# Kernel tuning notes

Measured on AMD Instinct MI355X. Metric: run time of the kernel, lower is better.

Reference implementation:

```python
import jax, jax.numpy as jnp
import numpy as np

N_GO, N_KE, D = 8000, 2000, 16
N_LAYERS, N_TISSUE, DRUG = 3, 512, 2048
B = 256


def _scatter_add(msgs, dst, n):
    # msgs: [B, E, D] -> [B, n, D], summing messages into destination nodes
    Bm, _, d = msgs.shape
    return jnp.zeros((Bm, n, d), msgs.dtype).at[:, dst, :].add(msgs)


def setup_inputs() -> dict:
    key = jax.random.key(0)
    ks = jax.random.split(key, 20)
    inp = {
        "x": jax.random.normal(ks[0], (B, N_GO + DRUG), jnp.float32),
        "go_ke_src": jax.random.randint(ks[1], (50000,), 0, N_GO),
        "go_ke_dst": jax.random.randint(ks[2], (50000,), 0, N_KE),
        "ke_ke_src": jax.random.randint(ks[3], (20000,), 0, N_KE),
        "ke_ke_dst": jax.random.randint(ks[4], (20000,), 0, N_KE),
        "tissue": jax.random.randint(ks[5], (N_TISSUE,), 0, N_KE),
    }
    def w(k, shape, fan_in):
        return jax.random.normal(k, shape, jnp.float32) / np.sqrt(fan_in)
    inp["W_dec"] = w(ks[6], (N_GO, D), 1.0)          # per-GO scalar->vector layer
    inp["b_dec"] = jnp.zeros((N_GO, D), jnp.float32)
    inp["W_g2k"] = w(ks[7], (D, D), D)
    inp["b_g2k"] = jnp.zeros((D,), jnp.float32)
    inp["W_kk"] = w(ks[8], (N_LAYERS, D, D), D)
    inp["b_kk"] = jnp.zeros((N_LAYERS, D), jnp.float32)
    inp["w_ke"] = w(ks[9], (D,), D)                   # node readout D->1
    inp["b_ke"] = jnp.zeros((), jnp.float32)
    inp["W_bio1"] = w(ks[10], (N_TISSUE, 256), N_TISSUE)
    inp["b_bio1"] = jnp.zeros((256,), jnp.float32)
    inp["W_bio2"] = w(ks[11], (256, 128), 256)
    inp["b_bio2"] = jnp.zeros((128,), jnp.float32)
    inp["W_drug1"] = w(ks[12], (DRUG, 512), DRUG)
    inp["b_drug1"] = jnp.zeros((512,), jnp.float32)
    inp["W_drug2"] = w(ks[13], (512, 128), 512)
    inp["b_drug2"] = jnp.zeros((128,), jnp.float32)
    inp["W_pred"] = w(ks[14], (256, 1), 256)
    inp["b_pred"] = jnp.zeros((1,), jnp.float32)
    return inp


def reference(x, go_ke_src, go_ke_dst, ke_ke_src, ke_ke_dst, tissue,
              W_dec, b_dec, W_g2k, b_g2k, W_kk, b_kk, w_ke, b_ke,
              W_bio1, b_bio1, W_bio2, b_bio2,
              W_drug1, b_drug1, W_drug2, b_drug2, W_pred, b_pred):
    # go_decode_layer: per-GO scalar -> D-dim node feature
    go = jnp.tanh(x[:, :-DRUG, None] * W_dec + b_dec)          # [B, N_GO, D]
    # go2ke: gather source GO features, scatter-add into KE nodes, transform
    ke = _scatter_add(go[:, go_ke_src, :], go_ke_dst, N_KE)    # [B, N_KE, D]
    ke = jnp.tanh(ke @ W_g2k + b_g2k)
    # ke2ke message-passing layers
    for l in range(W_kk.shape[0]):
        agg = _scatter_add(ke[:, ke_ke_src, :], ke_ke_dst, N_KE)
        ke = jnp.tanh((ke + agg) @ W_kk[l] + b_kk[l])
    # ke_layer: per-node readout D -> scalar
    ke = jnp.tanh(jnp.einsum('bnd,d->bn', ke, w_ke) + b_ke)    # [B, N_KE]
    # tissue gather + bio MLP head
    bio = ke[:, tissue]                                         # [B, N_TISSUE]
    bio = jax.nn.relu(bio @ W_bio1 + b_bio1)
    bio = jax.nn.relu(bio @ W_bio2 + b_bio2)
    # drug fingerprint MLP head
    drug = x[:, -DRUG:]
    drug = jax.nn.relu(drug @ W_drug1 + b_drug1)
    drug = jax.nn.relu(drug @ W_drug2 + b_drug2)
    # predictor on concatenated features
    comb = jnp.concatenate([bio, drug], axis=-1)                # [B, 256]
    return comb @ W_pred + b_pred                               # [B, 1]
```

## Files before the change

### kernel.cpp

```cpp
#include <hip/hip_runtime.h>
#include <hip/hip_bf16.h>
#include <cstdint>
#include <cstddef>

#define BATCH 256
#define NGO   8000
#define NKE   2000
#define DD    16
#define XCOLS 10048
#define NDRUG 2048
#define NT    512
#define NSLAB 8
#define SB    32
#define TANH_SCALE 2.885390081777926f

__device__ __forceinline__ float tanh_fast(float z) {
    float e = __builtin_amdgcn_exp2f(z * TANH_SCALE);
    float r = __builtin_amdgcn_rcpf(e + 1.0f);
    return fmaf(-2.0f, r, 1.0f);
}

__device__ __forceinline__ float rcp_core(float zp) {
    float e = __builtin_amdgcn_exp2f(zp);
    return __builtin_amdgcn_rcpf(e + 1.0f);
}

__device__ __forceinline__ void add4(float4& a, const float4 b) {
    a.x += b.x; a.y += b.y; a.z += b.z; a.w += b.w;
}

#define RFL(v) __builtin_amdgcn_readfirstlane(v)

__global__ void k_scan2(const int* __restrict__ cnt_go, const int* __restrict__ cnt_kk,
                        int* __restrict__ rp_go, int* __restrict__ rp_kk) {
    const int* cnt = blockIdx.x ? cnt_kk : cnt_go;
    int* rowptr    = blockIdx.x ? rp_kk  : rp_go;
    __shared__ int s[2048];
    int t = threadIdx.x;
    s[t]        = (t        < NKE) ? cnt[t]        : 0;
    s[t + 1024] = (t + 1024 < NKE) ? cnt[t + 1024] : 0;
    __syncthreads();
    for (int st = 1; st < 2048; st <<= 1) {
        int v0 = (t >= st) ? s[t - st] : 0;
        int v1 = s[t + 1024 - st];
        __syncthreads();
        s[t] += v0; s[t + 1024] += v1;
        __syncthreads();
    }
    if (t == 0) rowptr[0] = 0;
    rowptr[t + 1] = s[t];
    if (t + 1024 < NKE) rowptr[t + 1025] = s[t + 1024];
}

__global__ void k_fill2(const int* __restrict__ gs, const int* __restrict__ gdst,
                        const int* __restrict__ ks, const int* __restrict__ kdst,
                        int Eg, int Ek,
                        const int* __restrict__ rp_go, int* __restrict__ cur_go, int* __restrict__ col_go,
                        const int* __restrict__ rp_kk, int* __restrict__ cur_kk, int* __restrict__ col_kk) {
    int e = blockIdx.x * 256 + threadIdx.x;
    if (e < Eg) {
        int d = gdst[e];
        int p = atomicAdd(&cur_go[d], 1);
        col_go[rp_go[d] + p] = gs[e];
    } else if (e < Eg + Ek) {
        int e2 = e - Eg;
        int d = kdst[e2];
        int p = atomicAdd(&cur_kk[d], 1);
        col_kk[rp_kk[d] + p] = ks[e2];
    }
}

__global__ __launch_bounds__(256) void k_prep(const float* __restrict__ x,
                                              float* __restrict__ xT,
                                              float* __restrict__ xdT,
                                              const float* __restrict__ bd,
                                              float* __restrict__ bds,
                                              const int* __restrict__ gdst,
                                              const int* __restrict__ kdst,
                                              int* __restrict__ cnt_go,
                                              int* __restrict__ cnt_kk,
                                              int Eg, int Ek) {
    int bid = blockIdx.x;
    if (bid >= 1128) {
        int e = (bid - 1128) * 256 + threadIdx.x;
        if (e < Eg) atomicAdd(&cnt_go[gdst[e]], 1);
        else if (e < Eg + Ek) atomicAdd(&cnt_kk[kdst[e - Eg]], 1);
        return;
    }
    if (bid >= 628) {
        int i = (bid - 628) * 256 + threadIdx.x;
        bds[i] = bd[i] * TANH_SCALE;
        return;
    }
    __shared__ float tile[64][69];
    int c4 = threadIdx.x & 15, rr = threadIdx.x >> 4;
    int n0, b0;
    bool isgo = bid < 500;
    if (isgo) { n0 = (bid % 125) * 64; b0 = (bid / 125) * 64; }
    else      { int t = bid - 500; n0 = NGO + (t & 31) * 64; b0 = (t >> 5) * 64; }
#pragma unroll
    for (int i = 0; i < 4; i++) {
        int row = rr + i * 16;
        float4 v = *(const float4*)&x[(size_t)(b0 + row) * XCOLS + n0 + c4 * 4];
        tile[row][c4 * 4 + 0] = v.x; tile[row][c4 * 4 + 1] = v.y;
        tile[row][c4 * 4 + 2] = v.z; tile[row][c4 * 4 + 3] = v.w;
    }
    __syncthreads();
#pragma unroll
    for (int i = 0; i < 4; i++) {
        int nrow = rr + i * 16;
        float4 w;
        w.x = tile[c4 * 4 + 0][nrow]; w.y = tile[c4 * 4 + 1][nrow];
        w.z = tile[c4 * 4 + 2][nrow]; w.w = tile[c4 * 4 + 3][nrow];
        if (isgo) {
            w.x *= TANH_SCALE; w.y *= TANH_SCALE; w.z *= TANH_SCALE; w.w *= TANH_SCALE;
            *(float4*)&xT[(size_t)(n0 + nrow) * 256 + b0 + c4 * 4] = w;
        } else {
            *(float4*)&xdT[(size_t)(n0 - NGO + nrow) * 256 + b0 + c4 * 4] = w;
        }
    }
}

__global__ __launch_bounds__(128) void k_fuse(const float* __restrict__ xT,
                                              const int* __restrict__ rowptr,
                                              const int* __restrict__ col,
                                              const float* __restrict__ Wd,
                                              const float* __restrict__ bds,
                                              const float* __restrict__ W,
                                              const float* __restrict__ bias,
                                              float* __restrict__ ke) {
    __shared__ float pre[32 * 17];
    __shared__ float Ws[256];
    __shared__ float bs[16];
    int s = blockIdx.x & 7, n = blockIdx.x >> 3;
    int tid = threadIdx.x;
    Ws[tid] = W[tid]; Ws[tid + 128] = W[tid + 128];
    if (tid < 16) bs[tid] = bias[tid];
    int bloc = tid >> 2, d4 = tid & 3;
    int bglob = s * SB + bloc;

    int e   = RFL(rowptr[n]);
    int end = RFL(rowptr[n + 1]);
    float degF = (float)(end - e);
    float4 acc = make_float4(0, 0, 0, 0);
    for (; e + 3 < end; e += 4) {
        int s0 = RFL(col[e]);
        int s1 = RFL(col[e + 1]);
        int s2 = RFL(col[e + 2]);
        int s3 = RFL(col[e + 3]);
        float xv0 = (xT + (size_t)s0 * 256)[bglob];
        float xv1 = (xT + (size_t)s1 * 256)[bglob];
        float xv2 = (xT + (size_t)s2 * 256)[bglob];
        float xv3 = (xT + (size_t)s3 * 256)[bglob];
        float4 w0 = *(const float4*)(Wd  + (size_t)s0 * 16 + d4 * 4);
        float4 w1 = *(const float4*)(Wd  + (size_t)s1 * 16 + d4 * 4);
        float4 w2 = *(const float4*)(Wd  + (size_t)s2 * 16 + d4 * 4);
        float4 w3 = *(const float4*)(Wd  + (size_t)s3 * 16 + d4 * 4);
        float4 c0 = *(const float4*)(bds + (size_t)s0 * 16 + d4 * 4);
        float4 c1 = *(const float4*)(bds + (size_t)s1 * 16 + d4 * 4);
        float4 c2 = *(const float4*)(bds + (size_t)s2 * 16 + d4 * 4);
        float4 c3 = *(const float4*)(bds + (size_t)s3 * 16 + d4 * 4);
        acc.x += rcp_core(fmaf(xv0, w0.x, c0.x)) + rcp_core(fmaf(xv1, w1.x, c1.x))
               + rcp_core(fmaf(xv2, w2.x, c2.x)) + rcp_core(fmaf(xv3, w3.x, c3.x));
        acc.y += rcp_core(fmaf(xv0, w0.y, c0.y)) + rcp_core(fmaf(xv1, w1.y, c1.y))
               + rcp_core(fmaf(xv2, w2.y, c2.y)) + rcp_core(fmaf(xv3, w3.y, c3.y));
        acc.z += rcp_core(fmaf(xv0, w0.z, c0.z)) + rcp_core(fmaf(xv1, w1.z, c1.z))
               + rcp_core(fmaf(xv2, w2.z, c2.z)) + rcp_core(fmaf(xv3, w3.z, c3.z));
        acc.w += rcp_core(fmaf(xv0, w0.w, c0.w)) + rcp_core(fmaf(xv1, w1.w, c1.w))
               + rcp_core(fmaf(xv2, w2.w, c2.w)) + rcp_core(fmaf(xv3, w3.w, c3.w));
    }
    for (; e < end; ++e) {
        int s0 = RFL(col[e]);
        float xv0 = (xT + (size_t)s0 * 256)[bglob];
        float4 w0 = *(const float4*)(Wd  + (size_t)s0 * 16 + d4 * 4);
        float4 c0 = *(const float4*)(bds + (size_t)s0 * 16 + d4 * 4);
        acc.x += rcp_core(fmaf(xv0, w0.x, c0.x));
        acc.y += rcp_core(fmaf(xv0, w0.y, c0.y));
        acc.z += rcp_core(fmaf(xv0, w0.z, c0.z));
        acc.w += rcp_core(fmaf(xv0, w0.w, c0.w));
    }
    pre[bloc * 17 + d4 * 4 + 0] = fmaf(-2.0f, acc.x, degF);
    pre[bloc * 17 + d4 * 4 + 1] = fmaf(-2.0f, acc.y, degF);
    pre[bloc * 17 + d4 * 4 + 2] = fmaf(-2.0f, acc.z, degF);
    pre[bloc * 17 + d4 * 4 + 3] = fmaf(-2.0f, acc.w, degF);
    __syncthreads();

    float4 o;
    float* op = &o.x;
#pragma unroll
    for (int q = 0; q < 4; q++) {
        int dp = d4 * 4 + q;
        float a = bs[dp];
#pragma unroll
        for (int d = 0; d < 16; d++) a = fmaf(pre[bloc * 17 + d], Ws[d * 16 + dp], a);
        op[q] = tanh_fast(a);
    }
    *(float4*)&ke[((size_t)s * NKE + n) * 512 + bloc * 16 + d4 * 4] = o;
}

__global__ __launch_bounds__(128) void k_layer(const float* __restrict__ kin,
                                               const int* __restrict__ rowptr,
                                               const int* __restrict__ col,
                                               const float* __restrict__ W,
                                               const float* __restrict__ bias,
                                               float* __restrict__ kout) {
    __shared__ float pre[32 * 17];
    __shared__ float Ws[256];
    __shared__ float bs[16];
    int s = blockIdx.x & 7, n = blockIdx.x >> 3;
    int tid = threadIdx.x;
    Ws[tid] = W[tid]; Ws[tid + 128] = W[tid + 128];
    if (tid < 16) bs[tid] = bias[tid];
    int bloc = tid >> 2, d4 = tid & 3;
    const float* slab = kin + (size_t)s * NKE * 512;

    float4 acc = *(const float4*)(slab + (size_t)n * 512 + tid * 4);
    int e   = RFL(rowptr[n]);
    int end = RFL(rowptr[n + 1]);
    for (; e + 3 < end; e += 4) {
        int c0 = RFL(col[e]), c1 = RFL(col[e + 1]), c2 = RFL(col[e + 2]), c3 = RFL(col[e + 3]);
        float4 v0 = *(const float4*)(slab + (size_t)c0 * 512 + tid * 4);
        float4 v1 = *(const float4*)(slab + (size_t)c1 * 512 + tid * 4);
        float4 v2 = *(const float4*)(slab + (size_t)c2 * 512 + tid * 4);
        float4 v3 = *(const float4*)(slab + (size_t)c3 * 512 + tid * 4);
        add4(acc, v0); add4(acc, v1); add4(acc, v2); add4(acc, v3);
    }
    for (; e < end; ++e) {
        int c0 = RFL(col[e]);
        float4 v0 = *(const float4*)(slab + (size_t)c0 * 512 + tid * 4);
        add4(acc, v0);
    }
    pre[bloc * 17 + d4 * 4 + 0] = acc.x;
    pre[bloc * 17 + d4 * 4 + 1] = acc.y;
    pre[bloc * 17 + d4 * 4 + 2] = acc.z;
    pre[bloc * 17 + d4 * 4 + 3] = acc.w;
    __syncthreads();

    float4 o;
    float* op = &o.x;
#pragma unroll
    for (int q = 0; q < 4; q++) {
        int dp = d4 * 4 + q;
        float a = bs[dp];
#pragma unroll
        for (int d = 0; d < 16; d++) a = fmaf(pre[bloc * 17 + d], Ws[d * 16 + dp], a);
        op[q] = tanh_fast(a);
    }
    *(float4*)&kout[(size_t)s * NKE * 512 + (size_t)n * 512 + bloc * 16 + d4 * 4] = o;
}

__global__ __launch_bounds__(256) void k_kescalar(const float* __restrict__ ke,
                                                  const int* __restrict__ tissue,
                                                  const float* __restrict__ wke,
                                                  const float* __restrict__ bke,
                                                  float* __restrict__ bioT) {
    int t = blockIdx.x, b = threadIdx.x;
    int n = RFL(tissue[t]);
    int s = b >> 5, bloc = b & 31;
    const float4* kp = (const float4*)&ke[((size_t)s * NKE + n) * 512 + bloc * 16];
    const float4* wp = (const float4*)wke;
    float4 k0 = kp[0], k1 = kp[1], k2 = kp[2], k3 = kp[3];
    float4 w0 = wp[0], w1 = wp[1], w2 = wp[2], w3 = wp[3];
    float acc = bke[0];
    acc += k0.x * w0.x + k0.y * w0.y + k0.z * w0.z + k0.w * w0.w;
    acc += k1.x * w1.x + k1.y * w1.y + k1.z * w1.z + k1.w * w1.w;
    acc += k2.x * w2.x + k2.y * w2.y + k2.z * w2.z + k2.w * w2.w;
    acc += k3.x * w3.x + k3.y * w3.y + k3.z * w3.z + k3.w * w3.w;
    bioT[t * 256 + b] = tanh_fast(acc);
}

__global__ __launch_bounds__(256) void k_gemm(const float* __restrict__ A,
                                              const float* __restrict__ W,
                                              float* __restrict__ Cpart,
                                              int N, int Kper) {
    __shared__ float As[32][68];
    __shared__ float Ws[32][68];
    int tid = threadIdx.x;
    int tx = tid & 15, ty = tid >> 4;
    int jt = blockIdx.x * 64, bt = blockIdx.y * 64;
    int ks = blockIdx.z;
    int k0 = ks * Kper;

    float acc[4][4];
#pragma unroll
    for (int i = 0; i < 4; i++)
#pragma unroll
        for (int j = 0; j < 4; j++) acc[i][j] = 0.0f;

    for (int kc = 0; kc < Kper; kc += 32) {
#pragma unroll
        for (int i = 0; i < 8; i++) {
            int idx = tid + i * 256;
            int kk = idx >> 6, cc = idx & 63;
            As[kk][cc] = A[(size_t)(k0 + kc + kk) * 256 + bt + cc];
            Ws[kk][cc] = W[(size_t)(k0 + kc + kk) * N + jt + cc];
        }
        __syncthreads();
#pragma unroll 8
        for (int kk = 0; kk < 32; kk++) {
            float4 a = *(const float4*)&As[kk][tx * 4];
            float4 w = *(const float4*)&Ws[kk][ty * 4];
            acc[0][0] = fmaf(w.x, a.x, acc[0][0]); acc[0][1] = fmaf(w.x, a.y, acc[0][1]);
            acc[0][2] = fmaf(w.x, a.z, acc[0][2]); acc[0][3] = fmaf(w.x, a.w, acc[0][3]);
            acc[1][0] = fmaf(w.y, a.x, acc[1][0]); acc[1][1] = fmaf(w.y, a.y, acc[1][1]);
            acc[1][2] = fmaf(w.y, a.z, acc[1][2]); acc[1][3] = fmaf(w.y, a.w, acc[1][3]);
            acc[2][0] = fmaf(w.z, a.x, acc[2][0]); acc[2][1] = fmaf(w.z, a.y, acc[2][1]);
            acc[2][2] = fmaf(w.z, a.z, acc[2][2]); acc[2][3] = fmaf(w.z, a.w, acc[2][3]);
            acc[3][0] = fmaf(w.w, a.x, acc[3][0]); acc[3][1] = fmaf(w.w, a.y, acc[3][1]);
            acc[3][2] = fmaf(w.w, a.z, acc[3][2]); acc[3][3] = fmaf(w.w, a.w, acc[3][3]);
        }
        __syncthreads();
    }
#pragma unroll
    for (int jy = 0; jy < 4; jy++) {
        int j = jt + ty * 4 + jy;
        float4 v = make_float4(acc[jy][0], acc[jy][1], acc[jy][2], acc[jy][3]);
        *(float4*)&Cpart[((size_t)ks * N + j) * 256 + bt + tx * 4] = v;
    }
}

__global__ __launch_bounds__(256) void k_red(const float* __restrict__ Cpart,
                                             const float* __restrict__ bias,
                                             float* __restrict__ C, int N, int S) {
    int j = blockIdx.x, b = threadIdx.x;
    float acc = bias[j];
    for (int s = 0; s < S; s++) acc += Cpart[((size_t)s * N + j) * 256 + b];
    C[j * 256 + b] = fmaxf(acc, 0.0f);
}

__global__ __launch_bounds__(256) void k_final(const float* __restrict__ bio2T,
                                               const float* __restrict__ drug2T,
                                               const float* __restrict__ Wp,
                                               const float* __restrict__ bp,
                                               float* __restrict__ out) {
    int b = threadIdx.x;
    float acc = bp[0];
#pragma unroll 8
    for (int i = 0; i < 128; i++) acc = fmaf(bio2T[i * 256 + b], Wp[i], acc);
#pragma unroll 8
    for (int i = 0; i < 128; i++) acc = fmaf(drug2T[i * 256 + b], Wp[128 + i], acc);
    out[b] = acc;
}

extern "C" void kernel_launch(void* const* d_in, const int* in_sizes, int n_in,
                              void* d_out, int out_size, void* d_ws, size_t ws_size,
                              hipStream_t stream) {
    const float* x       = (const float*)d_in[0];
    const int*   go_src  = (const int*)d_in[1];
    const int*   go_dst  = (const int*)d_in[2];
    const int*   kk_src  = (const int*)d_in[3];
    const int*   kk_dst  = (const int*)d_in[4];
    const int*   tissue  = (const int*)d_in[5];
    const float* W_dec   = (const float*)d_in[6];
    const float* b_dec   = (const float*)d_in[7];
    const float* W_g2k   = (const float*)d_in[8];
    const float* b_g2k   = (const float*)d_in[9];
    const float* W_kk    = (const float*)d_in[10];
    const float* b_kk    = (const float*)d_in[11];
    const float* w_ke    = (const float*)d_in[12];
    const float* b_ke    = (const float*)d_in[13];
    const float* W_bio1  = (const float*)d_in[14];
    const float* b_bio1  = (const float*)d_in[15];
    const float* W_bio2  = (const float*)d_in[16];
    const float* b_bio2  = (const float*)d_in[17];
    const float* W_drug1 = (const float*)d_in[18];
    const float* b_drug1 = (const float*)d_in[19];
    const float* W_drug2 = (const float*)d_in[20];
    const float* b_drug2 = (const float*)d_in[21];
    const float* W_pred  = (const float*)d_in[22];
    const float* b_pred  = (const float*)d_in[23];
    float* out = (float*)d_out;

    const int E_GO = in_sizes[1];
    const int E_KK = in_sizes[3];

    char* wsb = (char*)d_ws;
    size_t off = 0;
    float* xT      = (float*)(wsb + off); off += (size_t)NGO * 256 * 4;
    float* ke_a    = (float*)(wsb + off); off += (size_t)NSLAB * NKE * 512 * 4;
    float* ke_b    = (float*)(wsb + off); off += (size_t)NSLAB * NKE * 512 * 4;
    float* bio_inT = (float*)(wsb + off); off += (size_t)NT * 256 * 4;
    float* bio1T   = (float*)(wsb + off); off += (size_t)256 * 256 * 4;
    float* bio2T   = (float*)(wsb + off); off += (size_t)128 * 256 * 4;
    float* xdT     = (float*)(wsb + off); off += (size_t)NDRUG * 256 * 4;
    float* drug1T  = (float*)(wsb + off); off += (size_t)512 * 256 * 4;
    float* drug2T  = (float*)(wsb + off); off += (size_t)128 * 256 * 4;
    float* bds     = (float*)(wsb + off); off += (size_t)NGO * 16 * 4;
    float* cpart   = (float*)(wsb + off); off += (size_t)8 * 512 * 256 * 4;
    int* cnt_go    = (int*)(wsb + off); off += 2048 * 4;
    int* cur_go    = (int*)(wsb + off); off += 2048 * 4;
    int* cnt_kk    = (int*)(wsb + off); off += 2048 * 4;
    int* cur_kk    = (int*)(wsb + off); off += 2048 * 4;
    int* rp_go     = (int*)(wsb + off); off += 2048 * 4;
    int* rp_kk     = (int*)(wsb + off); off += 2048 * 4;
    int* col_go    = (int*)(wsb + off); off += 50048 * 4;
    int* col_kk    = (int*)(wsb + off); off += 20048 * 4;

    hipMemsetAsync(cnt_go, 0, 4 * 2048 * 4, stream);

    int Etot = E_GO + E_KK;
    int histBlocks = (Etot + 255) / 256;

    k_prep<<<1128 + histBlocks, 256, 0, stream>>>(x, xT, xdT, b_dec, bds,
                                                  go_dst, kk_dst, cnt_go, cnt_kk, E_GO, E_KK);
    k_scan2<<<2, 1024, 0, stream>>>(cnt_go, cnt_kk, rp_go, rp_kk);
    k_fill2<<<histBlocks, 256, 0, stream>>>(go_src, go_dst, kk_src, kk_dst, E_GO, E_KK,
                                            rp_go, cur_go, col_go, rp_kk, cur_kk, col_kk);

    k_fuse<<<NKE * NSLAB, 128, 0, stream>>>(xT, rp_go, col_go, W_dec, bds, W_g2k, b_g2k, ke_a);
    k_layer<<<NKE * NSLAB, 128, 0, stream>>>(ke_a, rp_kk, col_kk, W_kk + 0 * 256, b_kk + 0 * 16, ke_b);
    k_layer<<<NKE * NSLAB, 128, 0, stream>>>(ke_b, rp_kk, col_kk, W_kk + 1 * 256, b_kk + 1 * 16, ke_a);
    k_layer<<<NKE * NSLAB, 128, 0, stream>>>(ke_a, rp_kk, col_kk, W_kk + 2 * 256, b_kk + 2 * 16, ke_b);
    k_kescalar<<<NT, 256, 0, stream>>>(ke_b, tissue, w_ke, b_ke, bio_inT);

    k_gemm<<<dim3(8, 4, 8), 256, 0, stream>>>(xdT, W_drug1, cpart, 512, 256);
    k_red<<<512, 256, 0, stream>>>(cpart, b_drug1, drug1T, 512, 8);
    k_gemm<<<dim3(2, 4, 8), 256, 0, stream>>>(drug1T, W_drug2, cpart, 128, 64);
    k_red<<<128, 256, 0, stream>>>(cpart, b_drug2, drug2T, 128, 8);

    k_gemm<<<dim3(4, 4, 8), 256, 0, stream>>>(bio_inT, W_bio1, cpart, 256, 64);
    k_red<<<256, 256, 0, stream>>>(cpart, b_bio1, bio1T, 256, 8);
    k_gemm<<<dim3(2, 4, 8), 256, 0, stream>>>(bio1T, W_bio2, cpart, 128, 32);
    k_red<<<128, 256, 0, stream>>>(cpart, b_bio2, bio2T, 128, 8);

    k_final<<<1, 256, 0, stream>>>(bio2T, drug2T, W_pred, b_pred, out);
}
```

Measured before the change: 224.6 us.

## Merge independent drug and bio head kernels into shared launches

Combines the tissue readout with the first drug GEMM, and pairs each split-K GEMM of one head with the reduction of the other head in a single launch, partitioned by block ID. Each stage gets its own partial-sum buffer so the interleaved stages do not overwrite each other. This cuts the launch count from nine to five and lets small independent grids fill the GPU together. In exchange it uses more workspace, and every block reserves the GEMM shared memory even when it only does light work.

Measured after the change: 222.1 us, median of 2. No clear change (-1.1%).

```diff
diff --git a/kernel.cpp b/kernel.cpp
--- a/kernel.cpp
+++ b/kernel.cpp
@@ -249,12 +249,12 @@
     *(float4*)&kout[(size_t)s * NKE * 512 + (size_t)n * 512 + bloc * 16 + d4 * 4] = o;
 }
 
-__global__ __launch_bounds__(256) void k_kescalar(const float* __restrict__ ke,
-                                                  const int* __restrict__ tissue,
-                                                  const float* __restrict__ wke,
-                                                  const float* __restrict__ bke,
-                                                  float* __restrict__ bioT) {
-    int t = blockIdx.x, b = threadIdx.x;
+__device__ __forceinline__ void dev_kescalar(int t, const float* __restrict__ ke,
+                                             const int* __restrict__ tissue,
+                                             const float* __restrict__ wke,
+                                             const float* __restrict__ bke,
+                                             float* __restrict__ bioT) {
+    int b = threadIdx.x;
     int n = RFL(tissue[t]);
     int s = b >> 5, bloc = b & 31;
     const float4* kp = (const float4*)&ke[((size_t)s * NKE + n) * 512 + bloc * 16];
@@ -269,16 +269,17 @@
     bioT[t * 256 + b] = tanh_fast(acc);
 }
 
-__global__ __launch_bounds__(256) void k_gemm(const float* __restrict__ A,
-                                              const float* __restrict__ W,
-                                              float* __restrict__ Cpart,
-                                              int N, int Kper) {
-    __shared__ float As[32][68];
-    __shared__ float Ws[32][68];
+__device__ __forceinline__ void dev_gemm(int bid, const float* __restrict__ A,
+                                         const float* __restrict__ W,
+                                         float* __restrict__ Cpart,
+                                         int N, int Kper, int gx,
+                                         float (*As)[68], float (*Ws)[68]) {
     int tid = threadIdx.x;
     int tx = tid & 15, ty = tid >> 4;
-    int jt = blockIdx.x * 64, bt = blockIdx.y * 64;
-    int ks = blockIdx.z;
+    int jx = bid % gx;
+    int by = (bid / gx) & 3;
+    int ks = bid / (gx * 4);
+    int jt = jx * 64, bt = by * 64;
     int k0 = ks * Kper;
 
     float acc[4][4];
@@ -319,13 +320,49 @@
     }
 }
 
+__device__ __forceinline__ void dev_red(int j, const float* __restrict__ Cpart,
+                                        const float* __restrict__ bias,
+                                        float* __restrict__ C, int N, int S) {
+    int b = threadIdx.x;
+    float acc = bias[j];
+    for (int s = 0; s < S; s++) acc += Cpart[((size_t)s * N + j) * 256 + b];
+    C[j * 256 + b] = fmaxf(acc, 0.0f);
+}
+
+__global__ __launch_bounds__(256) void k_kg(const float* __restrict__ ke,
+                                            const int* __restrict__ tissue,
+                                            const float* __restrict__ wke,
+                                            const float* __restrict__ bke,
+                                            float* __restrict__ bioT,
+                                            const float* __restrict__ A,
+                                            const float* __restrict__ W,
+                                            float* __restrict__ Cpart,
+                                            int N, int Kper, int gx, int nk) {
+    __shared__ float As[32][68];
+    __shared__ float Ws[32][68];
+    int bid = blockIdx.x;
+    if (bid < nk) dev_kescalar(bid, ke, tissue, wke, bke, bioT);
+    else          dev_gemm(bid - nk, A, W, Cpart, N, Kper, gx, As, Ws);
+}
+
+__global__ __launch_bounds__(256) void k_gr(const float* __restrict__ A,
+                                            const float* __restrict__ W,
+                                            float* __restrict__ Cpart,
+                                            int N, int Kper, int gx, int gB,
+                                            const float* __restrict__ Rcp,
+                                            const float* __restrict__ Rbias,
+                                            float* __restrict__ RC, int RN, int RS) {
+    __shared__ float As[32][68];
+    __shared__ float Ws[32][68];
+    int bid = blockIdx.x;
+    if (bid < gB) dev_gemm(bid, A, W, Cpart, N, Kper, gx, As, Ws);
+    else          dev_red(bid - gB, Rcp, Rbias, RC, RN, RS);
+}
+
 __global__ __launch_bounds__(256) void k_red(const float* __restrict__ Cpart,
                                              const float* __restrict__ bias,
                                              float* __restrict__ C, int N, int S) {
-    int j = blockIdx.x, b = threadIdx.x;
-    float acc = bias[j];
-    for (int s = 0; s < S; s++) acc += Cpart[((size_t)s * N + j) * 256 + b];
-    C[j * 256 + b] = fmaxf(acc, 0.0f);
+    dev_red(blockIdx.x, Cpart, bias, C, N, S);
 }
 
 __global__ __launch_bounds__(256) void k_final(const float* __restrict__ bio2T,
@@ -386,7 +423,10 @@
     float* drug1T  = (float*)(wsb + off); off += (size_t)512 * 256 * 4;
     float* drug2T  = (float*)(wsb + off); off += (size_t)128 * 256 * 4;
     float* bds     = (float*)(wsb + off); off += (size_t)NGO * 16 * 4;
-    float* cpart   = (float*)(wsb + off); off += (size_t)8 * 512 * 256 * 4;
+    float* cp_d1   = (float*)(wsb + off); off += (size_t)8 * 512 * 256 * 4;
+    float* cp_b1   = (float*)(wsb + off); off += (size_t)8 * 256 * 256 * 4;
+    float* cp_d2   = (float*)(wsb + off); off += (size_t)8 * 128 * 256 * 4;
+    float* cp_b2   = (float*)(wsb + off); off += (size_t)8 * 128 * 256 * 4;
     int* cnt_go    = (int*)(wsb + off); off += 2048 * 4;
     int* cur_go    = (int*)(wsb + off); off += 2048 * 4;
     int* cnt_kk    = (int*)(wsb + off); off += 2048 * 4;
@@ -411,17 +451,16 @@
     k_layer<<<NKE * NSLAB, 128, 0, stream>>>(ke_a, rp_kk, col_kk, W_kk + 0 * 256, b_kk + 0 * 16, ke_b);
     k_layer<<<NKE * NSLAB, 128, 0, stream>>>(ke_b, rp_kk, col_kk, W_kk + 1 * 256, b_kk + 1 * 16, ke_a);
     k_layer<<<NKE * NSLAB, 128, 0, stream>>>(ke_a, rp_kk, col_kk, W_kk + 2 * 256, b_kk + 2 * 16, ke_b);
-    k_kescalar<<<NT, 256, 0, stream>>>(ke_b, tissue, w_ke, b_ke, bio_inT);
-
-    k_gemm<<<dim3(8, 4, 8), 256, 0, stream>>>(xdT, W_drug1, cpart, 512, 256);
-    k_red<<<512, 256, 0, stream>>>(cpart, b_drug1, drug1T, 512, 8);
-    k_gemm<<<dim3(2, 4, 8), 256, 0, stream>>>(drug1T, W_drug2, cpart, 128, 64);
-    k_red<<<128, 256, 0, stream>>>(cpart, b_drug2, drug2T, 128, 8);
-
-    k_gemm<<<dim3(4, 4, 8), 256, 0, stream>>>(bio_inT, W_bio1, cpart, 256, 64);
-    k_red<<<256, 256, 0, stream>>>(cpart, b_bio1, bio1T, 256, 8);
-    k_gemm<<<dim3(2, 4, 8), 256, 0, stream>>>(bio1T, W_bio2, cpart, 128, 32);
-    k_red<<<128, 256, 0, stream>>>(cpart, b_bio2, bio2T, 128, 8);
+
+    k_kg<<<NT + 256, 256, 0, stream>>>(ke_b, tissue, w_ke, b_ke, bio_inT,
+                                       xdT, W_drug1, cp_d1, 512, 256, 8, NT);
+    k_gr<<<128 + 512, 256, 0, stream>>>(bio_inT, W_bio1, cp_b1, 256, 64, 4, 128,
+                                        cp_d1, b_drug1, drug1T, 512, 8);
+    k_gr<<<64 + 256, 256, 0, stream>>>(drug1T, W_drug2, cp_d2, 128, 64, 2, 64,
+                                       cp_b1, b_bio1, bio1T, 256, 8);
+    k_gr<<<64 + 128, 256, 0, stream>>>(bio1T, W_bio2, cp_b2, 128, 32, 2, 64,
+                                       cp_d2, b_drug2, drug2T, 128, 8);
+    k_red<<<128, 256, 0, stream>>>(cp_b2, b_bio2, bio2T, 128, 8);
 
     k_final<<<1, 256, 0, stream>>>(bio2T, drug2T, W_pred, b_pred, out);
 }
```

## Piggyback drug MLP GEMM and reduce blocks onto graph-layer kernel launches

Applied to the files above, without the earlier changes.

The drug-branch GEMMs and partial-sum reductions are folded into the fuse and ke2ke layer kernels as extra trailing blocks, each running a 128-thread version of the gemm or reduce body. This removes four separate launches from the serial chain and lets the independent drug work fill idle CUs next to the memory-bound gather kernels. The partial-sum buffers are split per stage so the stages cannot alias. The cost is larger shared memory in the fused kernels and GEMM tiles that now run on 128-thread blocks.

After: 230.0 us. 1.02x slower.

```diff
diff --git a/kernel.cpp b/kernel.cpp
--- a/kernel.cpp
+++ b/kernel.cpp
@@ -121,18 +121,98 @@
     }
 }
 
-__global__ __launch_bounds__(128) void k_fuse(const float* __restrict__ xT,
-                                              const int* __restrict__ rowptr,
-                                              const int* __restrict__ col,
-                                              const float* __restrict__ Wd,
-                                              const float* __restrict__ bds,
-                                              const float* __restrict__ W,
-                                              const float* __restrict__ bias,
-                                              float* __restrict__ ke) {
-    __shared__ float pre[32 * 17];
-    __shared__ float Ws[256];
-    __shared__ float bs[16];
-    int s = blockIdx.x & 7, n = blockIdx.x >> 3;
+__device__ __forceinline__ void gemm128_body(int bid, const float* __restrict__ A,
+                                             const float* __restrict__ W,
+                                             float* __restrict__ Cpart,
+                                             int N, int Kper, int gx,
+                                             float (*As)[36], float (*Ws)[68]) {
+    int tid = threadIdx.x;
+    int tx = tid & 7, ty = tid >> 3;
+    int jx = bid % gx;
+    int by = (bid / gx) & 7;
+    int ks = bid / (gx * 8);
+    int jt = jx * 64, bt = by * 32;
+    int k0 = ks * Kper;
+
+    float acc[4][4];
+#pragma unroll
+    for (int i = 0; i < 4; i++)
+#pragma unroll
+        for (int j = 0; j < 4; j++) acc[i][j] = 0.0f;
+
+    for (int kc = 0; kc < Kper; kc += 32) {
+#pragma unroll
+        for (int i = 0; i < 8; i++) {
+            int idx = tid + i * 128;
+            int kk = idx >> 5, cc = idx & 31;
+            As[kk][cc] = A[(size_t)(k0 + kc + kk) * 256 + bt + cc];
+        }
+#pragma unroll
+        for (int i = 0; i < 16; i++) {
+            int idx = tid + i * 128;
+            int kk = idx >> 6, cc = idx & 63;
+            Ws[kk][cc] = W[(size_t)(k0 + kc + kk) * N + jt + cc];
+        }
+        __syncthreads();
+#pragma unroll 8
+        for (int kk = 0; kk < 32; kk++) {
+            float4 a = *(const float4*)&As[kk][tx * 4];
+            float4 w = *(const float4*)&Ws[kk][ty * 4];
+            acc[0][0] = fmaf(w.x, a.x, acc[0][0]); acc[0][1] = fmaf(w.x, a.y, acc[0][1]);
+            acc[0][2] = fmaf(w.x, a.z, acc[0][2]); acc[0][3] = fmaf(w.x, a.w, acc[0][3]);
+            acc[1][0] = fmaf(w.y, a.x, acc[1][0]); acc[1][1] = fmaf(w.y, a.y, acc[1][1]);
+            acc[1][2] = fmaf(w.y, a.z, acc[1][2]); acc[1][3] = fmaf(w.y, a.w, acc[1][3]);
+            acc[2][0] = fmaf(w.z, a.x, acc[2][0]); acc[2][1] = fmaf(w.z, a.y, acc[2][1]);
+            acc[2][2] = fmaf(w.z, a.z, acc[2][2]); acc[2][3] = fmaf(w.z, a.w, acc[2][3]);
+            acc[3][0] = fmaf(w.w, a.x, acc[3][0]); acc[3][1] = fmaf(w.w, a.y, acc[3][1]);
+            acc[3][2] = fmaf(w.w, a.z, acc[3][2]); acc[3][3] = fmaf(w.w, a.w, acc[3][3]);
+        }
+        __syncthreads();
+    }
+#pragma unroll
+    for (int jy = 0; jy < 4; jy++) {
+        int j = jt + ty * 4 + jy;
+        float4 v = make_float4(acc[jy][0], acc[jy][1], acc[jy][2], acc[jy][3]);
+        *(float4*)&Cpart[((size_t)ks * N + j) * 256 + bt + tx * 4] = v;
+    }
+}
+
+__device__ __forceinline__ void red128_body(int j, const float* __restrict__ Cpart,
+                                            const float* __restrict__ bias,
+                                            float* __restrict__ C, int N, int S) {
+    int b = threadIdx.x;
+    float a0 = bias[j], a1 = a0;
+    for (int s = 0; s < S; s++) {
+        a0 += Cpart[((size_t)s * N + j) * 256 + b];
+        a1 += Cpart[((size_t)s * N + j) * 256 + b + 128];
+    }
+    C[j * 256 + b]       = fmaxf(a0, 0.0f);
+    C[j * 256 + b + 128] = fmaxf(a1, 0.0f);
+}
+
+__global__ __launch_bounds__(128) void k_fuse_g(const float* __restrict__ xT,
+                                                const int* __restrict__ rowptr,
+                                                const int* __restrict__ col,
+                                                const float* __restrict__ Wd,
+                                                const float* __restrict__ bds,
+                                                const float* __restrict__ W,
+                                                const float* __restrict__ bias,
+                                                float* __restrict__ ke,
+                                                const float* __restrict__ gA,
+                                                const float* __restrict__ gW,
+                                                float* __restrict__ gC,
+                                                int gN, int gKper, int ggx, int nFuse) {
+    __shared__ __align__(16) float shbuf[32 * 36 + 32 * 68];
+    int bid = blockIdx.x;
+    if (bid >= nFuse) {
+        gemm128_body(bid - nFuse, gA, gW, gC, gN, gKper, ggx,
+                     (float(*)[36])shbuf, (float(*)[68])(shbuf + 32 * 36));
+        return;
+    }
+    float* pre = shbuf;
+    float* Ws  = shbuf + 544;
+    float* bs  = shbuf + 800;
+    int s = bid & 7, n = bid >> 3;
     int tid = threadIdx.x;
     Ws[tid] = W[tid]; Ws[tid + 128] = W[tid + 128];
     if (tid < 16) bs[tid] = bias[tid];
@@ -198,16 +278,14 @@
     *(float4*)&ke[((size_t)s * NKE + n) * 512 + bloc * 16 + d4 * 4] = o;
 }
 
-__global__ __launch_bounds__(128) void k_layer(const float* __restrict__ kin,
-                                               const int* __restrict__ rowptr,
-                                               const int* __restrict__ col,
-                                               const float* __restrict__ W,
-                                               const float* __restrict__ bias,
-                                               float* __restrict__ kout) {
-    __shared__ float pre[32 * 17];
-    __shared__ float Ws[256];
-    __shared__ float bs[16];
-    int s = blockIdx.x & 7, n = blockIdx.x >> 3;
+__device__ __forceinline__ void layer_body(int bid, const float* __restrict__ kin,
+                                           const int* __restrict__ rowptr,
+                                           const int* __restrict__ col,
+                                           const float* __restrict__ W,
+                                           const float* __restrict__ bias,
+                                           float* __restrict__ kout,
+                                           float* pre, float* Ws, float* bs) {
+    int s = bid & 7, n = bid >> 3;
     int tid = threadIdx.x;
     Ws[tid] = W[tid]; Ws[tid + 128] = W[tid + 128];
     if (tid < 16) bs[tid] = bias[tid];
@@ -247,6 +325,42 @@
         op[q] = tanh_fast(a);
     }
     *(float4*)&kout[(size_t)s * NKE * 512 + (size_t)n * 512 + bloc * 16 + d4 * 4] = o;
+}
+
+__global__ __launch_bounds__(128) void k_layer_red(const float* __restrict__ kin,
+                                                   const int* __restrict__ rowptr,
+                                                   const int* __restrict__ col,
+                                                   const float* __restrict__ W,
+                                                   const float* __restrict__ bias,
+                                                   float* __restrict__ kout,
+                                                   const float* __restrict__ Rcp,
+                                                   const float* __restrict__ Rbias,
+                                                   float* __restrict__ RC, int RN, int RS,
+                                                   int nLayer) {
+    __shared__ __align__(16) float shbuf[816];
+    int bid = blockIdx.x;
+    if (bid >= nLayer) { red128_body(bid - nLayer, Rcp, Rbias, RC, RN, RS); return; }
+    layer_body(bid, kin, rowptr, col, W, bias, kout, shbuf, shbuf + 544, shbuf + 800);
+}
+
+__global__ __launch_bounds__(128) void k_layer_gemm(const float* __restrict__ kin,
+                                                    const int* __restrict__ rowptr,
+                                                    const int* __restrict__ col,
+                                                    const float* __restrict__ W,
+                                                    const float* __restrict__ bias,
+                                                    float* __restrict__ kout,
+                                                    const float* __restrict__ gA,
+                                                    const float* __restrict__ gW,
+                                                    float* __restrict__ gC,
+                                                    int gN, int gKper, int ggx, int nLayer) {
+    __shared__ __align__(16) float shbuf[32 * 36 + 32 * 68];
+    int bid = blockIdx.x;
+    if (bid >= nLayer) {
+        gemm128_body(bid - nLayer, gA, gW, gC, gN, gKper, ggx,
+                     (float(*)[36])shbuf, (float(*)[68])(shbuf + 32 * 36));
+        return;
+    }
+    layer_body(bid, kin, rowptr, col, W, bias, kout, shbuf, shbuf + 544, shbuf + 800);
 }
 
 __global__ __launch_bounds__(256) void k_kescalar(const float* __restrict__ ke,
@@ -386,7 +500,10 @@
     float* drug1T  = (float*)(wsb + off); off += (size_t)512 * 256 * 4;
     float* drug2T  = (float*)(wsb + off); off += (size_t)128 * 256 * 4;
     float* bds     = (float*)(wsb + off); off += (size_t)NGO * 16 * 4;
-    float* cpart   = (float*)(wsb + off); off += (size_t)8 * 512 * 256 * 4;
+    float* cp_d1   = (float*)(wsb + off); off += (size_t)8 * 512 * 256 * 4;
+    float* cp_b1   = (float*)(wsb + off); off += (size_t)8 * 256 * 256 * 4;
+    float* cp_d2   = (float*)(wsb + off); off += (size_t)8 * 128 * 256 * 4;
+    float* cp_b2   = (float*)(wsb + off); off += (size_t)8 * 128 * 256 * 4;
     int* cnt_go    = (int*)(wsb + off); off += 2048 * 4;
     int* cur_go    = (int*)(wsb + off); off += 2048 * 4;
     int* cnt_kk    = (int*)(wsb + off); off += 2048 * 4;
@@ -400,6 +517,7 @@
 
     int Etot = E_GO + E_KK;
     int histBlocks = (Etot + 255) / 256;
+    const int NFUSE = NKE * NSLAB;
 
     k_prep<<<1128 + histBlocks, 256, 0, stream>>>(x, xT, xdT, b_dec, bds,
                                                   go_dst, kk_dst, cnt_go, cnt_kk, E_GO, E_KK);
@@ -407,21 +525,23 @@
     k_fill2<<<histBlocks, 256, 0, stream>>>(go_src, go_dst, kk_src, kk_dst, E_GO, E_KK,
                                             rp_go, cur_go, col_go, rp_kk, cur_kk, col_kk);
 
-    k_fuse<<<NKE * NSLAB, 128, 0, stream>>>(xT, rp_go, col_go, W_dec, bds, W_g2k, b_g2k, ke_a);
-    k_layer<<<NKE * NSLAB, 128, 0, stream>>>(ke_a, rp_kk, col_kk, W_kk + 0 * 256, b_kk + 0 * 16, ke_b);
-    k_layer<<<NKE * NSLAB, 128, 0, stream>>>(ke_b, rp_kk, col_kk, W_kk + 1 * 256, b_kk + 1 * 16, ke_a);
-    k_layer<<<NKE * NSLAB, 128, 0, stream>>>(ke_a, rp_kk, col_kk, W_kk + 2 * 256, b_kk + 2 * 16, ke_b);
+    k_fuse_g<<<NFUSE + 512, 128, 0, stream>>>(xT, rp_go, col_go, W_dec, bds, W_g2k, b_g2k, ke_a,
+                                              xdT, W_drug1, cp_d1, 512, 256, 8, NFUSE);
+    k_layer_red<<<NFUSE + 512, 128, 0, stream>>>(ke_a, rp_kk, col_kk,
+                                                 W_kk + 0 * 256, b_kk + 0 * 16, ke_b,
+                                                 cp_d1, b_drug1, drug1T, 512, 8, NFUSE);
+    k_layer_gemm<<<NFUSE + 128, 128, 0, stream>>>(ke_b, rp_kk, col_kk,
+                                                  W_kk + 1 * 256, b_kk + 1 * 16, ke_a,
+                                                  drug1T, W_drug2, cp_d2, 128, 64, 2, NFUSE);
+    k_layer_red<<<NFUSE + 128, 128, 0, stream>>>(ke_a, rp_kk, col_kk,
+                                                 W_kk + 2 * 256, b_kk + 2 * 16, ke_b,
+                                                 cp_d2, b_drug2, drug2T, 128, 8, NFUSE);
+
     k_kescalar<<<NT, 256, 0, stream>>>(ke_b, tissue, w_ke, b_ke, bio_inT);
-
-    k_gemm<<<dim3(8, 4, 8), 256, 0, stream>>>(xdT, W_drug1, cpart, 512, 256);
-    k_red<<<512, 256, 0, stream>>>(cpart, b_drug1, drug1T, 512, 8);
-    k_gemm<<<dim3(2, 4, 8), 256, 0, stream>>>(drug1T, W_drug2, cpart, 128, 64);
-    k_red<<<128, 256, 0, stream>>>(cpart, b_drug2, drug2T, 128, 8);
-
-    k_gemm<<<dim3(4, 4, 8), 256, 0, stream>>>(bio_inT, W_bio1, cpart, 256, 64);
-    k_red<<<256, 256, 0, stream>>>(cpart, b_bio1, bio1T, 256, 8);
-    k_gemm<<<dim3(2, 4, 8), 256, 0, stream>>>(bio1T, W_bio2, cpart, 128, 32);
-    k_red<<<128, 256, 0, stream>>>(cpart, b_bio2, bio2T, 128, 8);
+    k_gemm<<<dim3(4, 4, 8), 256, 0, stream>>>(bio_inT, W_bio1, cp_b1, 256, 64);
+    k_red<<<256, 256, 0, stream>>>(cp_b1, b_bio1, bio1T, 256, 8);
+    k_gemm<<<dim3(2, 4, 8), 256, 0, stream>>>(bio1T, W_bio2, cp_b2, 128, 32);
+    k_red<<<128, 256, 0, stream>>>(cp_b2, b_bio2, bio2T, 128, 8);
 
     k_final<<<1, 256, 0, stream>>>(bio2T, drug2T, W_pred, b_pred, out);
 }
```
